# Kernel tuning notes

Hardware: AMD Instinct MI355X
Metric: run time of the kernel (lower is better)

Reference implementation:

```python
import jax, jax.numpy as jnp
import numpy as np

M, K = 64, 8192                     # decode batch of 64 tokens, hidden 8192
ALL_OUT = (8192, 1024, 1024)        # merged Q, K, V (GQA)
N = sum(ALL_OUT)                    # 10240


def setup_inputs() -> dict:
    key = jax.random.key(0)
    k1, k2, k3, k4 = jax.random.split(key, 4)
    x = jax.random.normal(k1, (M, K), dtype=jnp.float16)
    # int8 quantized merged weight, [out_features, in_features]
    weight = jax.random.randint(k2, (N, K), -127, 128, dtype=jnp.int8)
    # per-output-channel dequant scale, [out_features, 1], small positive values
    scale = jax.random.uniform(k3, (N, 1), dtype=jnp.float32) * 0.01 + 1e-3
    bias = jax.random.normal(k4, (N,), dtype=jnp.float16)
    return {"x": x, "weight": weight, "scale": scale, "bias": bias}


def reference(x, weight, scale, bias):
    """w8a8 linear: per-token dynamic int8 quant of x, int8 GEMM against
    per-channel-quantized weight, fused dequant (x_scale * w_scale) + bias."""
    xf = x.astype(jnp.float32)
    # per-token symmetric quantization of activations
    x_scale = jnp.max(jnp.abs(xf), axis=-1, keepdims=True) / 127.0  # [M, 1]
    xq = jnp.clip(jnp.round(xf / x_scale), -127.0, 127.0)           # [M, K]
    acc = jnp.einsum('mk,nk->mn', xq, weight.astype(jnp.float32))   # [M, N]
    out = acc * x_scale * scale[:, 0][None, :] + bias.astype(jnp.float32)
    return out.astype(x.dtype)
```

## Files before the change

kernel.cpp:

```cpp
#include <hip/hip_runtime.h>

#define M_DIM 64
#define K_DIM 8192
#define N_DIM 10240
#define KSPLIT 8
#define KBLK (K_DIM / KSPLIT)
#define KSTEP 128
#define NCHUNK (KBLK / KSTEP)
#define NTILE 64

typedef __attribute__((ext_vector_type(8))) short short8;
typedef __attribute__((ext_vector_type(4))) float f32x4;
typedef __attribute__((ext_vector_type(4))) int i32x4;

static __device__ __forceinline__ ushort f2bf_trunc(float f) {
    return (ushort)(__float_as_uint(f) >> 16);
}

__global__ __launch_bounds__(256) void quant_kernel(
    const float* __restrict__ x,
    ushort* __restrict__ xq,
    float* __restrict__ xscale) {
    const int m = blockIdx.x;
    const int tid = threadIdx.x;
    const float4* xrow = (const float4*)(x + m * K_DIM);
    float4 c[8];
    float mx = 0.f;
#pragma unroll
    for (int i = 0; i < 8; ++i) {
        c[i] = xrow[i * 256 + tid];
        mx = fmaxf(mx, fmaxf(fmaxf(fabsf(c[i].x), fabsf(c[i].y)),
                             fmaxf(fabsf(c[i].z), fabsf(c[i].w))));
    }
#pragma unroll
    for (int off = 32; off; off >>= 1) mx = fmaxf(mx, __shfl_xor(mx, off));
    __shared__ float wmax[4];
    if ((tid & 63) == 0) wmax[tid >> 6] = mx;
    __syncthreads();
    mx = fmaxf(fmaxf(wmax[0], wmax[1]), fmaxf(wmax[2], wmax[3]));
    const float s = mx / 127.0f;
    if (tid == 0) xscale[m] = s;

    ushort4* qrow = (ushort4*)(xq + m * K_DIM);
#pragma unroll
    for (int i = 0; i < 8; ++i) {
        float q0 = fminf(fmaxf(rintf(c[i].x / s), -127.f), 127.f);
        float q1 = fminf(fmaxf(rintf(c[i].y / s), -127.f), 127.f);
        float q2 = fminf(fmaxf(rintf(c[i].z / s), -127.f), 127.f);
        float q3 = fminf(fmaxf(rintf(c[i].w / s), -127.f), 127.f);
        ushort4 o;
        o.x = f2bf_trunc(q0);
        o.y = f2bf_trunc(q1);
        o.z = f2bf_trunc(q2);
        o.w = f2bf_trunc(q3);
        qrow[i * 256 + tid] = o;
    }
}

__global__ __launch_bounds__(256, 2) void gemm_kernel(
    const ushort* __restrict__ xq,
    const int* __restrict__ W,
    float* __restrict__ partials) {
    const int tid = threadIdx.x;
    const int w = tid >> 6;
    const int lane = tid & 63;
    const int r16 = lane & 15;
    const int kgrp = lane >> 4;
    const int n0 = blockIdx.x * NTILE;
    const int kb = blockIdx.y;
    const int k0 = kb * KBLK;

    __shared__ __align__(16) ushort Abuf[2][NTILE * KSTEP];
    __shared__ __align__(16) ushort Bbuf[2][NTILE * KSTEP];

    i32x4 aB[8];
    short8 aA[4];

#define ISSUE_B(c)                                                             \
    {                                                                          \
        const int* base = W + k0 + (c) * KSTEP + (lane & 31) * 4;              \
        _Pragma("unroll") for (int i = 0; i < 8; ++i) {                        \
            const int row = n0 + w * 16 + i * 2 + (lane >> 5);                 \
            aB[i] = *(const i32x4*)(base + (size_t)row * K_DIM);               \
        }                                                                      \
    }
#define ISSUE_A(c)                                                             \
    {                                                                          \
        const ushort* base = xq + k0 + (c) * KSTEP + (lane & 15) * 8;          \
        _Pragma("unroll") for (int i = 0; i < 4; ++i) {                        \
            const int row = w * 16 + i * 4 + (lane >> 4);                      \
            aA[i] = *(const short8*)(base + row * K_DIM);                      \
        }                                                                      \
    }
#define WRITE_A(bufi)                                                          \
    {                                                                          \
        _Pragma("unroll") for (int i = 0; i < 4; ++i) {                        \
            const int row = w * 16 + i * 4 + (lane >> 4);                      \
            const int off = ((lane & 15) * 16) ^ ((row & 7) << 4);             \
            *(short8*)((char*)&Abuf[bufi][row * KSTEP] + off) = aA[i];         \
        }                                                                      \
    }
#define WRITE_B(bufi)                                                          \
    {                                                                          \
        _Pragma("unroll") for (int i = 0; i < 8; ++i) {                        \
            const int row = w * 16 + i * 2 + (lane >> 5);                      \
            ushort4 h;                                                         \
            h.x = f2bf_trunc((float)aB[i][0]);                                 \
            h.y = f2bf_trunc((float)aB[i][1]);                                 \
            h.z = f2bf_trunc((float)aB[i][2]);                                 \
            h.w = f2bf_trunc((float)aB[i][3]);                                 \
            const int off = ((lane & 31) * 8) ^ ((row & 7) << 4);              \
            *(ushort4*)((char*)&Bbuf[bufi][row * KSTEP] + off) = h;            \
        }                                                                      \
    }
#define COMPUTE(bufi)                                                          \
    {                                                                          \
        _Pragma("unroll") for (int ks = 0; ks < 4; ++ks) {                     \
            const int swz = (ks * 64 + kgrp * 16) ^ ((r16 & 7) << 4);          \
            short8 bfrag = *(const short8*)(                                   \
                (char*)&Bbuf[bufi][(w * 16 + r16) * KSTEP] + swz);             \
            _Pragma("unroll") for (int mt = 0; mt < 4; ++mt) {                 \
                short8 afrag = *(const short8*)(                               \
                    (char*)&Abuf[bufi][(mt * 16 + r16) * KSTEP] + swz);        \
                acc[mt] = __builtin_amdgcn_mfma_f32_16x16x32_bf16(             \
                    afrag, bfrag, acc[mt], 0, 0, 0);                           \
            }                                                                  \
        }                                                                      \
    }

    f32x4 acc[4];
#pragma unroll
    for (int i = 0; i < 4; ++i) acc[i] = (f32x4){0.f, 0.f, 0.f, 0.f};

    ISSUE_B(0)
    ISSUE_A(0)
    WRITE_A(0)
    WRITE_B(0)
    __syncthreads();
    ISSUE_B(1)
    ISSUE_A(1)

#pragma unroll
    for (int c = 0; c < NCHUNK; ++c) {
        COMPUTE(c & 1);
        if (c < NCHUNK - 1) {
            __syncthreads();
            WRITE_A((c + 1) & 1)
            WRITE_B((c + 1) & 1)
            if (c + 2 < NCHUNK) {
                ISSUE_B(c + 2)
                ISSUE_A(c + 2)
            }
            __syncthreads();
        }
    }

    __syncthreads();
    float* Cl = (float*)&Abuf[0][0];
#pragma unroll
    for (int mt = 0; mt < 4; ++mt)
#pragma unroll
        for (int j = 0; j < 4; ++j)
            Cl[(mt * 16 + kgrp * 4 + j) * 64 + w * 16 + r16] = acc[mt][j];
    __syncthreads();
    float* pb = partials + (size_t)kb * (M_DIM * N_DIM);
#pragma unroll
    for (int i = 0; i < 4; ++i) {
        const int idx = tid + 256 * i;
        const int m = idx >> 4;
        const int ch = idx & 15;
        *(f32x4*)(pb + m * N_DIM + n0 + ch * 4) = ((const f32x4*)Cl)[idx];
    }
#undef ISSUE_B
#undef ISSUE_A
#undef WRITE_A
#undef WRITE_B
#undef COMPUTE
}

__global__ __launch_bounds__(256) void reduce_kernel(
    const float* __restrict__ partials,
    const float* __restrict__ xscale,
    const float* __restrict__ wscale,
    const float* __restrict__ bias,
    float* __restrict__ out) {
    const int idx = blockIdx.x * 256 + threadIdx.x;
    const int m = idx / (N_DIM / 4);
    const int c = idx - m * (N_DIM / 4);
    const f32x4* P = (const f32x4*)partials;
    f32x4 s = (f32x4){0.f, 0.f, 0.f, 0.f};
#pragma unroll
    for (int p = 0; p < KSPLIT; ++p)
        s += P[((size_t)p * M_DIM + m) * (N_DIM / 4) + c];
    f32x4 ws = ((const f32x4*)wscale)[c];
    f32x4 bs = ((const f32x4*)bias)[c];
    const float xs = xscale[m];
    ((f32x4*)out)[idx] = s * xs * ws + bs;
}

extern "C" void kernel_launch(void* const* d_in, const int* in_sizes, int n_in,
                              void* d_out, int out_size, void* d_ws, size_t ws_size,
                              hipStream_t stream) {
    const float* x = (const float*)d_in[0];
    const int* W = (const int*)d_in[1];
    const float* wscale = (const float*)d_in[2];
    const float* bias = (const float*)d_in[3];
    float* out = (float*)d_out;

    float* xscale = (float*)d_ws;
    ushort* xq = (ushort*)((char*)d_ws + 4096);
    float* partials = (float*)((char*)d_ws + 2097152);

    quant_kernel<<<M_DIM, 256, 0, stream>>>(x, xq, xscale);
    gemm_kernel<<<dim3(N_DIM / NTILE, KSPLIT), 256, 0, stream>>>(xq, W, partials);
    reduce_kernel<<<(M_DIM * N_DIM / 4) / 256, 256, 0, stream>>>(
        partials, xscale, wscale, bias, out);
}
```

Before: 87.74 us.

## Shrink N tile to 16 and split-K to 2 to cut partial traffic

Changes the GEMM decomposition from 64-wide N tiles with 8-way split-K to 16-wide N tiles with 2-way split-K. Each wave now owns one 16-row M slice, and the epilogue writes accumulators directly instead of staging them through shared memory. The reduce kernel sums only two partials. This removes most of the fp32 partial write and read traffic, at the cost of reloading the activation tile for every 16 output columns and issuing narrower, less coalesced output stores.

```diff
diff --git a/kernel.cpp b/kernel.cpp
--- a/kernel.cpp
+++ b/kernel.cpp
@@ -3,11 +3,11 @@
 #define M_DIM 64
 #define K_DIM 8192
 #define N_DIM 10240
-#define KSPLIT 8
+#define KSPLIT 2
 #define KBLK (K_DIM / KSPLIT)
 #define KSTEP 128
 #define NCHUNK (KBLK / KSTEP)
-#define NTILE 64
+#define NTILE 16
 
 typedef __attribute__((ext_vector_type(8))) short short8;
 typedef __attribute__((ext_vector_type(4))) float f32x4;
@@ -57,7 +57,7 @@
     }
 }
 
-__global__ __launch_bounds__(256, 2) void gemm_kernel(
+__global__ __launch_bounds__(256, 4) void gemm_kernel(
     const ushort* __restrict__ xq,
     const int* __restrict__ W,
     float* __restrict__ partials) {
@@ -70,19 +70,19 @@
     const int kb = blockIdx.y;
     const int k0 = kb * KBLK;
 
-    __shared__ __align__(16) ushort Abuf[2][NTILE * KSTEP];
+    __shared__ __align__(16) ushort Abuf[2][M_DIM * KSTEP];
     __shared__ __align__(16) ushort Bbuf[2][NTILE * KSTEP];
 
-    i32x4 aB[8];
+    i32x4 aB[2];
     short8 aA[4];
 
 #define ISSUE_B(c)                                                             \
     {                                                                          \
-        const int* base = W + k0 + (c) * KSTEP + (lane & 31) * 4;              \
-        _Pragma("unroll") for (int i = 0; i < 8; ++i) {                        \
-            const int row = n0 + w * 16 + i * 2 + (lane >> 5);                 \
-            aB[i] = *(const i32x4*)(base + (size_t)row * K_DIM);               \
-        }                                                                      \
+        const int* base =                                                      \
+            W + k0 + (c) * KSTEP + (size_t)(n0 + (tid >> 4)) * K_DIM +         \
+            (tid & 15) * 8;                                                    \
+        aB[0] = *(const i32x4*)(base);                                         \
+        aB[1] = *(const i32x4*)(base + 4);                                     \
     }
 #define ISSUE_A(c)                                                             \
     {                                                                          \
@@ -102,35 +102,29 @@
     }
 #define WRITE_B(bufi)                                                          \
     {                                                                          \
-        _Pragma("unroll") for (int i = 0; i < 8; ++i) {                        \
-            const int row = w * 16 + i * 2 + (lane >> 5);                      \
-            ushort4 h;                                                         \
-            h.x = f2bf_trunc((float)aB[i][0]);                                 \
-            h.y = f2bf_trunc((float)aB[i][1]);                                 \
-            h.z = f2bf_trunc((float)aB[i][2]);                                 \
-            h.w = f2bf_trunc((float)aB[i][3]);                                 \
-            const int off = ((lane & 31) * 8) ^ ((row & 7) << 4);              \
-            *(ushort4*)((char*)&Bbuf[bufi][row * KSTEP] + off) = h;            \
+        const int row = tid >> 4;                                              \
+        short8 h;                                                              \
+        _Pragma("unroll") for (int i = 0; i < 4; ++i) {                        \
+            h[i] = (short)f2bf_trunc((float)aB[0][i]);                         \
+            h[4 + i] = (short)f2bf_trunc((float)aB[1][i]);                     \
         }                                                                      \
+        const int off = ((tid & 15) * 16) ^ ((row & 7) << 4);                  \
+        *(short8*)((char*)&Bbuf[bufi][row * KSTEP] + off) = h;                 \
     }
 #define COMPUTE(bufi)                                                          \
     {                                                                          \
         _Pragma("unroll") for (int ks = 0; ks < 4; ++ks) {                     \
             const int swz = (ks * 64 + kgrp * 16) ^ ((r16 & 7) << 4);          \
             short8 bfrag = *(const short8*)(                                   \
-                (char*)&Bbuf[bufi][(w * 16 + r16) * KSTEP] + swz);             \
-            _Pragma("unroll") for (int mt = 0; mt < 4; ++mt) {                 \
-                short8 afrag = *(const short8*)(                               \
-                    (char*)&Abuf[bufi][(mt * 16 + r16) * KSTEP] + swz);        \
-                acc[mt] = __builtin_amdgcn_mfma_f32_16x16x32_bf16(             \
-                    afrag, bfrag, acc[mt], 0, 0, 0);                           \
-            }                                                                  \
+                (char*)&Bbuf[bufi][r16 * KSTEP] + swz);                        \
+            short8 afrag = *(const short8*)(                                   \
+                (char*)&Abuf[bufi][(w * 16 + r16) * KSTEP] + swz);             \
+            acc = __builtin_amdgcn_mfma_f32_16x16x32_bf16(                     \
+                afrag, bfrag, acc, 0, 0, 0);                                   \
         }                                                                      \
     }
 
-    f32x4 acc[4];
-#pragma unroll
-    for (int i = 0; i < 4; ++i) acc[i] = (f32x4){0.f, 0.f, 0.f, 0.f};
+    f32x4 acc = (f32x4){0.f, 0.f, 0.f, 0.f};
 
     ISSUE_B(0)
     ISSUE_A(0)
@@ -155,21 +149,11 @@
         }
     }
 
-    __syncthreads();
-    float* Cl = (float*)&Abuf[0][0];
-#pragma unroll
-    for (int mt = 0; mt < 4; ++mt)
-#pragma unroll
-        for (int j = 0; j < 4; ++j)
-            Cl[(mt * 16 + kgrp * 4 + j) * 64 + w * 16 + r16] = acc[mt][j];
-    __syncthreads();
     float* pb = partials + (size_t)kb * (M_DIM * N_DIM);
 #pragma unroll
-    for (int i = 0; i < 4; ++i) {
-        const int idx = tid + 256 * i;
-        const int m = idx >> 4;
-        const int ch = idx & 15;
-        *(f32x4*)(pb + m * N_DIM + n0 + ch * 4) = ((const f32x4*)Cl)[idx];
+    for (int j = 0; j < 4; ++j) {
+        const int m = w * 16 + kgrp * 4 + j;
+        pb[m * N_DIM + n0 + r16] = acc[j];
     }
 #undef ISSUE_B
 #undef ISSUE_A
@@ -188,10 +172,7 @@
     const int m = idx / (N_DIM / 4);
     const int c = idx - m * (N_DIM / 4);
     const f32x4* P = (const f32x4*)partials;
-    f32x4 s = (f32x4){0.f, 0.f, 0.f, 0.f};
-#pragma unroll
-    for (int p = 0; p < KSPLIT; ++p)
-        s += P[((size_t)p * M_DIM + m) * (N_DIM / 4) + c];
+    f32x4 s = P[idx] + P[(M_DIM * N_DIM / 4) + idx];
     f32x4 ws = ((const f32x4*)wscale)[c];
     f32x4 bs = ((const f32x4*)bias)[c];
     const float xs = xscale[m];
```

Result: slower. 91.80 us (+4.6%).
